# Kernel optimization log

Hardware: AMD Instinct MI355X
Metric: run time of the kernel (lower is better)

## Reference

```python
import jax, jax.numpy as jnp
import numpy as np
from jax import lax

B, N, C = 8, 16384, 128
HEADS, FF, KS = 8, 3.0, 5
HD = C // HEADS

def setup_inputs() -> dict:
    key = jax.random.key(0)
    ks = jax.random.split(key, 10)
    r = lambda k, s, sc=0.02: jax.random.normal(k, s, dtype=jnp.float32) * sc
    return {
        "x": jax.random.normal(ks[0], (B, N, C), dtype=jnp.float32),
        "Wq": r(ks[1], (C, C)),
        "Wkv": r(ks[2], (C, C)),
        "Wproj": r(ks[3], (C, C)),
        "bproj": jnp.zeros((C,), jnp.float32),
        "w_g": jax.random.normal(ks[4], (C, 1), dtype=jnp.float32),
        "scale": r(ks[5], (1, 1, C), 0.1),
        "pos_enc": r(ks[6], (1, N, C), 0.02),
        "dwc_w": r(ks[7], (HD, 1, KS, KS), 0.1),
        "dwc_b": jnp.zeros((HD,), jnp.float32),
        "H": 128,
        "W": 128,
    }

def _l2(a, axis):
    return jnp.sqrt(jnp.sum(a * a, axis=axis, keepdims=True))

def reference(x, Wq, Wkv, Wproj, bproj, w_g, scale, pos_enc, dwc_w, dwc_b, H, W):
    b, n_tok, c = x.shape
    scale_factor = HD ** (-0.5)
    q = x @ Wq.T                      # (B,N,C)
    k = x @ Wkv.T + pos_enc           # (B,N,C)  sr_ratio=1 path
    s = jax.nn.softplus(scale)
    q = (jax.nn.relu(q) + 1e-6) / s
    k = (jax.nn.relu(k) + 1e-6) / s
    qn, kn = _l2(q, -1), _l2(k, -1)
    q = q ** FF
    k = k ** FF
    q = q / _l2(q, -1) * qn
    k = k / _l2(k, -1) * kn
    A = (q @ w_g) * scale_factor      # (B,N,1)
    A = A / jnp.maximum(_l2(A, 1), 1e-12)  # F.normalize over dim=1
    G = jnp.sum(A * q, axis=1)        # (B,C)
    xg = G[:, None, :] * k            # (B,N,C)
    qh = q.reshape(b, n_tok, HEADS, HD).transpose(0, 2, 1, 3)  # (B,h,N,d)
    kh = k.reshape(b, n_tok, HEADS, HD).transpose(0, 2, 1, 3)
    z = 1.0 / (jnp.einsum('bhnd,bhd->bhn', qh, kh.mean(axis=2)) + 1e-6)
    xh = xg.reshape(b, n_tok, HEADS, HD).transpose(0, 2, 1, 3) * z[..., None]
    xo = xh.transpose(0, 2, 1, 3).reshape(b, n_tok, c)
    # faithful second transpose+reshape (memory reinterpretation in the source)
    xo = xo.transpose(0, 2, 1).reshape(b, n_tok, c)
    kimg = kh.reshape(b * HEADS, H, W, HD).transpose(0, 3, 1, 2)  # (B*h,d,H,W)
    pad = KS // 2
    conv = lax.conv_general_dilated(kimg, dwc_w, (1, 1), [(pad, pad), (pad, pad)],
                                    dimension_numbers=('NCHW', 'OIHW', 'NCHW'),
                                    feature_group_count=HD)
    conv = conv + dwc_b[None, :, None, None]
    xo = xo + conv.reshape(b, c, n_tok).transpose(0, 2, 1)
    return xo @ Wproj.T + bproj
```

## Files before the change

### kernel.cpp

```cpp
#include <hip/hip_runtime.h>
#include <hip/hip_bf16.h>

#define BB 8
#define NN 16384
#define CC 128

typedef __attribute__((ext_vector_type(8))) short bf16x8;
typedef __attribute__((ext_vector_type(4))) short short4v;
typedef __attribute__((ext_vector_type(4))) float f32x4;

__device__ __forceinline__ unsigned short f2bf(float f) {
    union { float f; unsigned u; } v; v.f = f;
    unsigned r = v.u + 0x7fffu + ((v.u >> 16) & 1u);
    return (unsigned short)(r >> 16);
}
__device__ __forceinline__ float bf2f(unsigned short h) {
    union { unsigned u; float f; } v; v.u = ((unsigned)h) << 16;
    return v.f;
}
__device__ __forceinline__ void split_trunc(float f, short& hi, short& lo) {
    union { float f; unsigned u; } v; v.f = f;
    const unsigned short hu = (unsigned short)(v.u >> 16);
    union { unsigned u; float f; } hf; hf.u = ((unsigned)hu) << 16;
    union { float f; unsigned u; } r; r.f = f - hf.f;
    hi = (short)hu;
    lo = (short)(r.u >> 16);
}

__global__ __launch_bounds__(256) void wprep_kernel(
    const float* __restrict__ Wq, const float* __restrict__ Wkv,
    const float* __restrict__ Wp, const float* __restrict__ scale,
    unsigned short* __restrict__ whi, unsigned short* __restrict__ wlo,
    float* __restrict__ sps)
{
    const int bid = blockIdx.x;
    if (bid == 48) {
        if (threadIdx.x < 128)
            sps[threadIdx.x] = 1.f / log1pf(expf(scale[threadIdx.x]));
        return;
    }
    const int mat = bid >> 4;
    const float* src = (mat == 0) ? Wq : ((mat == 1) ? Wkv : Wp);
    const int off = (bid & 15) * 1024 + threadIdx.x * 4;
    const float4 v = *(const float4*)(src + off);
    float f[4] = {v.x, v.y, v.z, v.w};
    short4v hv, lv;
#pragma unroll
    for (int j = 0; j < 4; ++j) {
        short h, lo2;
        split_trunc(f[j], h, lo2);
        hv[j] = h; lv[j] = lo2;
    }
    *(short4v*)(whi + mat * 16384 + off) = hv;
    *(short4v*)(wlo + mat * 16384 + off) = lv;
}

__global__ __launch_bounds__(256, 1) void qk_mfma_kernel(
    const float* __restrict__ x, const unsigned short* __restrict__ whi,
    const unsigned short* __restrict__ wlo, const float* __restrict__ w_g,
    const float* __restrict__ sps, const float* __restrict__ pos_enc,
    unsigned short* __restrict__ qout, unsigned short* __restrict__ kout,
    unsigned short* __restrict__ ktout, float* __restrict__ partial)
{
    __shared__ __align__(16) char wsm[131072];
    __shared__ float wpart[4][257];
    __shared__ float apl[128];

    const int tid  = threadIdx.x;
    const int w    = tid >> 6;
    const int l    = tid & 63;
    const int blk  = blockIdx.x;
    const int tok0 = blk * 128;
    const int tokb = (blk & 127) * 128;

    bf16x8 xh[2][4], xl[2][4];
#pragma unroll
    for (int n = 0; n < 2; ++n) {
        const int r = w * 32 + n * 16 + (l & 15);
        const float* rowp = x + (tok0 + r) * 128 + (l >> 4) * 8;
#pragma unroll
        for (int kt = 0; kt < 4; ++kt) {
            const f32x4 a = *(const f32x4*)(rowp + kt * 32);
            const f32x4 b = *(const f32x4*)(rowp + kt * 32 + 4);
            const float f[8] = {a[0], a[1], a[2], a[3], b[0], b[1], b[2], b[3]};
            bf16x8 hv, lv;
#pragma unroll
            for (int j = 0; j < 8; ++j) {
                short h, lo2;
                split_trunc(f[j], h, lo2);
                hv[j] = h; lv[j] = lo2;
            }
            xh[n][kt] = hv; xl[n][kt] = lv;
        }
    }

#pragma unroll
    for (int it = 0; it < 32; ++it) {
        const int flat = it * 256 + tid;
        const int arr  = flat >> 11;
        const int c    = (flat >> 4) & 127;
        const int g    = flat & 15;
        const unsigned short* src = ((arr & 1) ? wlo : whi)
                                  + ((arr >> 1) ? 16384 : 0) + c * 128 + g * 8;
        const int dst = arr * 32768 + c * 256 + ((g * 16) ^ ((c & 7) << 4));
        *(bf16x8*)(wsm + dst) = *(const bf16x8*)src;
    }
    __syncthreads();

    const int crow = (l >> 4) * 4;
    f32x4 accq[8][2], acck[8][2];
#pragma unroll
    for (int m = 0; m < 8; ++m)
#pragma unroll
        for (int n = 0; n < 2; ++n) { accq[m][n] = (f32x4)0.f; acck[m][n] = (f32x4)0.f; }

#pragma unroll
    for (int m = 0; m < 8; ++m) {
        const int c = m * 16 + (l & 15);
        const int sw = (c & 7) << 4;
        bf16x8 aqh[4], aql[4], akh[4], akl[4];
#pragma unroll
        for (int kt = 0; kt < 4; ++kt) {
            const int fo = c * 256 + ((kt * 64 + (l >> 4) * 16) ^ sw);
            aqh[kt] = *(const bf16x8*)(wsm + fo);
            aql[kt] = *(const bf16x8*)(wsm + 32768 + fo);
            akh[kt] = *(const bf16x8*)(wsm + 65536 + fo);
            akl[kt] = *(const bf16x8*)(wsm + 98304 + fo);
        }
#pragma unroll
        for (int n = 0; n < 2; ++n)
#pragma unroll
            for (int kt = 0; kt < 4; ++kt) {
                accq[m][n] = __builtin_amdgcn_mfma_f32_16x16x32_bf16(aqh[kt], xh[n][kt], accq[m][n], 0, 0, 0);
                acck[m][n] = __builtin_amdgcn_mfma_f32_16x16x32_bf16(akh[kt], xh[n][kt], acck[m][n], 0, 0, 0);
                accq[m][n] = __builtin_amdgcn_mfma_f32_16x16x32_bf16(aqh[kt], xl[n][kt], accq[m][n], 0, 0, 0);
                acck[m][n] = __builtin_amdgcn_mfma_f32_16x16x32_bf16(akh[kt], xl[n][kt], acck[m][n], 0, 0, 0);
                accq[m][n] = __builtin_amdgcn_mfma_f32_16x16x32_bf16(aql[kt], xh[n][kt], accq[m][n], 0, 0, 0);
                acck[m][n] = __builtin_amdgcn_mfma_f32_16x16x32_bf16(akl[kt], xh[n][kt], acck[m][n], 0, 0, 0);
            }
    }
    __syncthreads();

    {
#pragma unroll
        for (int m = 0; m < 8; ++m) {
            const float4 is4 = *(const float4*)(sps + m * 16 + crow);
            const float is[4] = {is4.x, is4.y, is4.z, is4.w};
#pragma unroll
            for (int n = 0; n < 2; ++n)
#pragma unroll
                for (int j = 0; j < 4; ++j)
                    accq[m][n][j] = (fmaxf(accq[m][n][j], 0.f) + 1e-6f) * is[j];
        }
        float fqn[2];
#pragma unroll
        for (int n = 0; n < 2; ++n) {
            float s2 = 0.f, s6 = 0.f;
#pragma unroll
            for (int m = 0; m < 8; ++m)
#pragma unroll
                for (int j = 0; j < 4; ++j) {
                    const float v = accq[m][n][j], v2 = v * v;
                    s2 += v2; s6 += v2 * v2 * v2;
                }
            s2 += __shfl_xor(s2, 16); s6 += __shfl_xor(s6, 16);
            s2 += __shfl_xor(s2, 32); s6 += __shfl_xor(s6, 32);
            fqn[n] = sqrtf(s2 / s6);
        }
#pragma unroll
        for (int m = 0; m < 8; ++m)
#pragma unroll
            for (int n = 0; n < 2; ++n)
#pragma unroll
                for (int j = 0; j < 4; ++j) {
                    const float v = accq[m][n][j];
                    accq[m][n][j] = v * v * v * fqn[n];
                }
        float d0 = 0.f, d1 = 0.f;
#pragma unroll
        for (int m = 0; m < 8; ++m) {
            const float4 wgv = *(const float4*)(w_g + m * 16 + crow);
#pragma unroll
            for (int j = 0; j < 4; ++j) {
                const float wg = (j == 0) ? wgv.x : (j == 1) ? wgv.y : (j == 2) ? wgv.z : wgv.w;
                d0 += accq[m][0][j] * wg;
                d1 += accq[m][1][j] * wg;
            }
        }
        d0 += __shfl_xor(d0, 16); d0 += __shfl_xor(d0, 32);
        d1 += __shfl_xor(d1, 16); d1 += __shfl_xor(d1, 32);
        const float ap0 = 0.25f * d0, ap1 = 0.25f * d1;

        float ssa = ap0 * ap0 + ap1 * ap1;
        ssa += __shfl_xor(ssa, 1); ssa += __shfl_xor(ssa, 2);
        ssa += __shfl_xor(ssa, 4); ssa += __shfl_xor(ssa, 8);
        if (l == 0) wpart[w][256] = ssa;
        if (l < 16) { apl[w * 32 + l] = ap0; apl[w * 32 + 16 + l] = ap1; }

        float g4[4] = {0.f, 0.f, 0.f, 0.f};
#pragma unroll
        for (int n = 0; n < 2; ++n) {
            const int t = l & 15;
            const int rb = w * 8192 + t * 512;
#pragma unroll
            for (int m = 0; m < 8; ++m) {
                const int ad = rb + (((m * 16 + crow) * 4) ^ ((t & 7) << 4));
                *(f32x4*)(wsm + ad) = accq[m][n];
            }
            asm volatile("s_waitcnt lgkmcnt(0)" ::: "memory");
#pragma unroll
            for (int j = 0; j < 8; ++j) {
                const int fid = j * 64 + l;
                const int row = fid >> 5;
                const int c4  = fid & 31;
                const int rb3 = w * 8192 + row * 512;
                const f32x4 v = *(f32x4*)(wsm + rb3 + ((c4 * 16) ^ ((row & 7) << 4)));
                const float apv = apl[w * 32 + n * 16 + row];
                short4v qv;
#pragma unroll
                for (int i = 0; i < 4; ++i) {
                    g4[i] += apv * v[i];
                    qv[i] = (short)f2bf(v[i]);
                }
                *(short4v*)(qout + (tok0 + w * 32 + n * 16 + row) * 128 + c4 * 4) = qv;
            }
        }
#pragma unroll
        for (int i = 0; i < 4; ++i) g4[i] += __shfl_xor(g4[i], 32);
        if (l < 32) {
#pragma unroll
            for (int i = 0; i < 4; ++i) wpart[w][(l & 31) * 4 + i] = g4[i];
        }
    }

    {
#pragma unroll
        for (int m = 0; m < 8; ++m) {
            const float4 is4 = *(const float4*)(sps + m * 16 + crow);
            const float is[4] = {is4.x, is4.y, is4.z, is4.w};
#pragma unroll
            for (int n = 0; n < 2; ++n) {
                const int t = tokb + w * 32 + n * 16 + (l & 15);
                const float4 p = *(const float4*)(pos_enc + t * 128 + m * 16 + crow);
                const float pe[4] = {p.x, p.y, p.z, p.w};
#pragma unroll
                for (int j = 0; j < 4; ++j)
                    acck[m][n][j] = (fmaxf(acck[m][n][j] + pe[j], 0.f) + 1e-6f) * is[j];
            }
        }
        float fkn[2];
#pragma unroll
        for (int n = 0; n < 2; ++n) {
            float s2 = 0.f, s6 = 0.f;
#pragma unroll
            for (int m = 0; m < 8; ++m)
#pragma unroll
                for (int j = 0; j < 4; ++j) {
                    const float v = acck[m][n][j], v2 = v * v;
                    s2 += v2; s6 += v2 * v2 * v2;
                }
            s2 += __shfl_xor(s2, 16); s6 += __shfl_xor(s6, 16);
            s2 += __shfl_xor(s2, 32); s6 += __shfl_xor(s6, 32);
            fkn[n] = sqrtf(s2 / s6);
        }
#pragma unroll
        for (int m = 0; m < 8; ++m)
#pragma unroll
            for (int n = 0; n < 2; ++n)
#pragma unroll
                for (int j = 0; j < 4; ++j) {
                    const float v = acck[m][n][j];
                    acck[m][n][j] = v * v * v * fkn[n];
                }
        float ks4[4] = {0.f, 0.f, 0.f, 0.f};
#pragma unroll
        for (int n = 0; n < 2; ++n) {
            const int t = l & 15;
            const int rb = w * 8192 + t * 512;
#pragma unroll
            for (int m = 0; m < 8; ++m) {
                const int ad = rb + (((m * 16 + crow) * 4) ^ ((t & 7) << 4));
                *(f32x4*)(wsm + ad) = acck[m][n];
            }
            asm volatile("s_waitcnt lgkmcnt(0)" ::: "memory");
#pragma unroll
            for (int j = 0; j < 8; ++j) {
                const int fid = j * 64 + l;
                const int row = fid >> 5;
                const int c4  = fid & 31;
                const int rb3 = w * 8192 + row * 512;
                const f32x4 v = *(f32x4*)(wsm + rb3 + ((c4 * 16) ^ ((row & 7) << 4)));
                short4v kv;
#pragma unroll
                for (int i = 0; i < 4; ++i) {
                    ks4[i] += v[i];
                    kv[i] = (short)f2bf(v[i]);
                }
                *(short4v*)(kout + (tok0 + w * 32 + n * 16 + row) * 128 + c4 * 4) = kv;
            }
        }
#pragma unroll
        for (int i = 0; i < 4; ++i) ks4[i] += __shfl_xor(ks4[i], 32);
        if (l < 32) {
#pragma unroll
            for (int i = 0; i < 4; ++i) wpart[w][128 + (l & 31) * 4 + i] = ks4[i];
        }
    }

    __syncthreads();
#pragma unroll
    for (int m = 0; m < 8; ++m)
#pragma unroll
        for (int n = 0; n < 2; ++n)
#pragma unroll
            for (int j = 0; j < 4; ++j) {
                const int ch = m * 16 + crow + j;
                const int tl = w * 32 + n * 16 + (l & 15);
                *(unsigned short*)(wsm + ch * 264 + tl * 2) = f2bf(acck[m][n][j]);
            }
    __syncthreads();
    {
        const int bb = blk >> 7;
        unsigned* ktp = (unsigned*)ktout;
#pragma unroll
        for (int it = 0; it < 32; ++it) {
            const int idx = it * 256 + tid;
            const int row = idx >> 6;
            const int col = idx & 63;
            const unsigned v = *(unsigned*)(wsm + row * 264 + col * 4);
            ktp[(size_t)(bb * 128 + row) * 8192 + (blk & 127) * 64 + col] = v;
        }
    }

    __syncthreads();
    float* pblk = partial + blk * 257;
    if (tid < 128) {
        pblk[tid] = wpart[0][tid] + wpart[1][tid] + wpart[2][tid] + wpart[3][tid];
        pblk[128 + tid] = wpart[0][128 + tid] + wpart[1][128 + tid] +
                          wpart[2][128 + tid] + wpart[3][128 + tid];
    } else if (tid == 128) {
        pblk[256] = wpart[0][256] + wpart[1][256] + wpart[2][256] + wpart[3][256];
    }
}

__global__ __launch_bounds__(256) void reduce_kernel(
    const float* __restrict__ partial, float* __restrict__ G,
    float* __restrict__ kbar)
{
    const int b = blockIdx.x;
    const int tid = threadIdx.x;
    __shared__ float tmp[4];

    float ssa = (tid < 128) ? partial[(b * 128 + tid) * 257 + 256] : 0.f;
#pragma unroll
    for (int o = 32; o >= 1; o >>= 1) ssa += __shfl_xor(ssa, o);
    if ((tid & 63) == 0) tmp[tid >> 6] = ssa;
    __syncthreads();
    const float anorm = fmaxf(sqrtf(tmp[0] + tmp[1] + tmp[2] + tmp[3]), 1e-12f);
    const float inv_a = 1.f / anorm;

    if (tid < 128) {
        float g = 0.f;
        for (int t = 0; t < 128; ++t)
            g += partial[(b * 128 + t) * 257 + tid];
        G[b * 128 + tid] = g * inv_a;
    } else {
        const int c2 = tid - 128;
        float s = 0.f;
        for (int t = 0; t < 128; ++t)
            s += partial[(b * 128 + t) * 257 + 128 + c2];
        kbar[b * 128 + c2] = s * (1.f / 16384.f);
    }
}

__global__ __launch_bounds__(256) void z_kernel(
    const unsigned short* __restrict__ q, const float* __restrict__ kbar,
    float* __restrict__ z)
{
    const int bid = blockIdx.x;
    const int b   = bid >> 8;
    const int tg  = bid & 255;
    const int tid = threadIdx.x;
    const int t   = tid >> 2;
    const int qt  = tid & 3;
    const int tok = tg * 64 + t;

    const unsigned short* qp = q + ((size_t)b * NN + tok) * 128 + qt * 32;
    const float* kb = kbar + b * 128 + qt * 32;

    float dot0 = 0.f, dot1 = 0.f;
#pragma unroll
    for (int c = 0; c < 4; ++c) {
        const short4v q4a = *(const short4v*)(qp + c * 8);
        const short4v q4b = *(const short4v*)(qp + c * 8 + 4);
        const float4 k4a = *(const float4*)(kb + c * 8);
        const float4 k4b = *(const float4*)(kb + c * 8 + 4);
        float d = bf2f((unsigned short)q4a[0]) * k4a.x + bf2f((unsigned short)q4a[1]) * k4a.y +
                  bf2f((unsigned short)q4a[2]) * k4a.z + bf2f((unsigned short)q4a[3]) * k4a.w +
                  bf2f((unsigned short)q4b[0]) * k4b.x + bf2f((unsigned short)q4b[1]) * k4b.y +
                  bf2f((unsigned short)q4b[2]) * k4b.z + bf2f((unsigned short)q4b[3]) * k4b.w;
        if (c < 2) dot0 += d; else dot1 += d;
    }
    z[((size_t)b * 8 + qt * 2) * NN + tok]     = 1.f / (dot0 + 1e-6f);
    z[((size_t)b * 8 + qt * 2 + 1) * NN + tok] = 1.f / (dot1 + 1e-6f);
}

__global__ __launch_bounds__(256, 2) void scp_kernel(
    float* __restrict__ out, const unsigned short* __restrict__ kbuf,
    const unsigned short* __restrict__ kt, const float* __restrict__ z,
    const float* __restrict__ G,
    const unsigned short* __restrict__ whi, const unsigned short* __restrict__ wlo,
    const float* __restrict__ bp, const float* __restrict__ dwc_w,
    const float* __restrict__ dwc_b)
{
    __shared__ __align__(16) char smem[65536];
    __shared__ float wct[25][16];
    __shared__ float bi[16];
    __shared__ float Gs;

    const int tid  = threadIdx.x;
    const int bid0 = blockIdx.x;
    const int bid  = (bid0 & 7) * 128 + (bid0 >> 3);
    const int cc   = bid & 127;
    const int b    = bid >> 7;
    const int n0   = bid * 128;

    for (int i = tid; i < 400; i += 256)
        wct[i >> 4][i & 15] = dwc_w[(i & 15) * 25 + (i >> 4)];
    if (tid < 16) bi[tid] = dwc_b[tid];
    if (tid == 0) Gs = G[b * 128 + cc];
    __syncthreads();

    const int l  = tid & 31;
    const int xg = tid >> 5;
    const int dbase = (l & 3) * 4;

    float4 acc[16];
#pragma unroll
    for (int i = 0; i < 16; ++i) acc[i] = make_float4(0.f, 0.f, 0.f, 0.f);

#pragma unroll
    for (int dy = 0; dy < 5; ++dy) {
        const int yy = cc + dy - 2;
        if (yy < 0 || yy > 127) continue;
        const unsigned short* rowb = kbuf + (b * NN + yy * 128) * CC + l * 4;
        float4 rowv[20];
#pragma unroll
        for (int xi = 0; xi < 20; ++xi) {
            const int xx = xg * 16 - 2 + xi;
            if (xx >= 0 && xx < 128) {
                const short4v kv4 = *(const short4v*)(rowb + xx * CC);
                rowv[xi] = make_float4(bf2f((unsigned short)kv4[0]),
                                       bf2f((unsigned short)kv4[1]),
                                       bf2f((unsigned short)kv4[2]),
                                       bf2f((unsigned short)kv4[3]));
            } else {
                rowv[xi] = make_float4(0.f, 0.f, 0.f, 0.f);
            }
        }
#pragma unroll
        for (int dx = 0; dx < 5; ++dx) {
            const float4 wv = *(const float4*)(&wct[dy * 5 + dx][dbase]);
#pragma unroll
            for (int i = 0; i < 16; ++i) {
                acc[i].x += wv.x * rowv[i + dx].x;
                acc[i].y += wv.y * rowv[i + dx].y;
                acc[i].z += wv.z * rowv[i + dx].z;
                acc[i].w += wv.w * rowv[i + dx].w;
            }
        }
    }

    const float Gcc = Gs;
    const unsigned short* kub = kt + ((size_t)b * 128 + cc) * NN;
    const float* zr = z + ((size_t)b * 8 + (cc >> 4)) * NN;
    const float4 b4 = *(const float4*)(&bi[dbase]);
#pragma unroll
    for (int i = 0; i < 16; ++i) {
        const int r = xg * 16 + i;
        const int toks = r * 128 + l * 4;
        const short4v ku4 = *(const short4v*)(kub + toks);
        const float4 z4 = *(const float4*)(zr + toks);
        const float zz[4] = {z4.x, z4.y, z4.z, z4.w};
        float f[4];
        const float av[4] = {acc[i].x, acc[i].y, acc[i].z, acc[i].w};
        const float bv[4] = {b4.x, b4.y, b4.z, b4.w};
#pragma unroll
        for (int c = 0; c < 4; ++c)
            f[c] = Gcc * bf2f((unsigned short)ku4[c]) * zz[c] + av[c] + bv[c];
        short4v hv, lv;
#pragma unroll
        for (int j = 0; j < 4; ++j) {
            short h, lo2;
            split_trunc(f[j], h, lo2);
            hv[j] = h; lv[j] = lo2;
        }
        const int ad = r * 256 + (((l >> 1) * 16) ^ ((r & 7) << 4)) + (l & 1) * 8;
        *(short4v*)(smem + ad) = hv;
        *(short4v*)(smem + 32768 + ad) = lv;
    }
    __syncthreads();

    const int w  = tid >> 6;
    const int ll = tid & 63;
    bf16x8 xh[2][4], xl[2][4];
    {
        const int lg16 = (ll >> 4) * 16;
#pragma unroll
        for (int n = 0; n < 2; ++n) {
            const int r = w * 32 + n * 16 + (ll & 15);
            const int rb = r * 256;
            const int sw = (r & 7) << 4;
#pragma unroll
            for (int kt2 = 0; kt2 < 4; ++kt2) {
                const int ad = rb + ((kt2 * 64 + lg16) ^ sw);
                xh[n][kt2] = *(bf16x8*)(smem + ad);
                xl[n][kt2] = *(bf16x8*)(smem + 32768 + ad);
            }
        }
    }
    const int crow = (ll >> 4) * 4;
    f32x4 pacc[8][2];
#pragma unroll
    for (int m = 0; m < 8; ++m)
#pragma unroll
        for (int n = 0; n < 2; ++n) pacc[m][n] = (f32x4)0.f;

#pragma unroll
    for (int m = 0; m < 8; ++m) {
        const int c = m * 16 + (ll & 15);
        bf16x8 ah[4], al[4];
#pragma unroll
        for (int kt2 = 0; kt2 < 4; ++kt2) {
            const int off = 32768 + c * 128 + kt2 * 32 + (ll >> 4) * 8;
            ah[kt2] = *(const bf16x8*)(whi + off);
            al[kt2] = *(const bf16x8*)(wlo + off);
        }
#pragma unroll
        for (int n = 0; n < 2; ++n)
#pragma unroll
            for (int kt2 = 0; kt2 < 4; ++kt2) {
                pacc[m][n] = __builtin_amdgcn_mfma_f32_16x16x32_bf16(ah[kt2], xh[n][kt2], pacc[m][n], 0, 0, 0);
                pacc[m][n] = __builtin_amdgcn_mfma_f32_16x16x32_bf16(ah[kt2], xl[n][kt2], pacc[m][n], 0, 0, 0);
                pacc[m][n] = __builtin_amdgcn_mfma_f32_16x16x32_bf16(al[kt2], xh[n][kt2], pacc[m][n], 0, 0, 0);
            }
    }

#pragma unroll
    for (int m = 0; m < 8; ++m) {
        const float4 bv = *(const float4*)(bp + m * 16 + crow);
        const float bb[4] = {bv.x, bv.y, bv.z, bv.w};
#pragma unroll
        for (int n = 0; n < 2; ++n)
#pragma unroll
            for (int j = 0; j < 4; ++j) pacc[m][n][j] += bb[j];
    }
    __syncthreads();
#pragma unroll
    for (int n = 0; n < 2; ++n) {
        const int t = n * 16 + (ll & 15);
        const int rb = w * 8192 + (t & 15) * 512 + ((t >= 16) ? 32768 : 0);
#pragma unroll
        for (int m = 0; m < 8; ++m) {
            const int ad = rb + (((m * 16 + crow) * 4) ^ ((t & 7) << 4));
            *(f32x4*)(smem + ad) = pacc[m][n];
        }
    }
    asm volatile("s_waitcnt lgkmcnt(0)" ::: "memory");
#pragma unroll
    for (int j = 0; j < 16; ++j) {
        const int fid = j * 64 + ll;
        const int row = fid >> 5;
        const int c4 = fid & 31;
        const int rb = w * 8192 + (row & 15) * 512 + ((row >= 16) ? 32768 : 0);
        const f32x4 v = *(f32x4*)(smem + rb + ((c4 * 16) ^ ((row & 7) << 4)));
        *(f32x4*)(out + (n0 + w * 32 + row) * 128 + c4 * 4) = v;
    }
}

extern "C" void kernel_launch(void* const* d_in, const int* in_sizes, int n_in,
                              void* d_out, int out_size, void* d_ws, size_t ws_size,
                              hipStream_t stream)
{
    const float* x       = (const float*)d_in[0];
    const float* Wq      = (const float*)d_in[1];
    const float* Wkv     = (const float*)d_in[2];
    const float* Wproj   = (const float*)d_in[3];
    const float* bproj   = (const float*)d_in[4];
    const float* w_g     = (const float*)d_in[5];
    const float* scale   = (const float*)d_in[6];
    const float* pos_enc = (const float*)d_in[7];
    const float* dwc_w   = (const float*)d_in[8];
    const float* dwc_b   = (const float*)d_in[9];
    float* out = (float*)d_out;

    char* ws = (char*)d_ws;
    unsigned short* qbuf = (unsigned short*)(ws);
    unsigned short* kbuf = (unsigned short*)(ws + 33554432);
    unsigned short* ktbuf= (unsigned short*)(ws + 67108864);
    float* partial = (float*)(ws + 100663296);
    float* G       = (float*)(ws + 101715968);
    float* kbar    = (float*)(ws + 101720064);
    unsigned short* whi = (unsigned short*)(ws + 101724160);
    unsigned short* wlo = (unsigned short*)(ws + 101822464);
    float* sps     = (float*)(ws + 101920768);
    float* zbuf    = (float*)(ws + 101921280);

    wprep_kernel<<<dim3(49), dim3(256), 0, stream>>>(
        Wq, Wkv, Wproj, scale, whi, wlo, sps);
    qk_mfma_kernel<<<dim3(1024), dim3(256), 0, stream>>>(
        x, whi, wlo, w_g, sps, pos_enc, qbuf, kbuf, ktbuf, partial);
    reduce_kernel<<<dim3(8), dim3(256), 0, stream>>>(partial, G, kbar);
    z_kernel<<<dim3(2048), dim3(256), 0, stream>>>(qbuf, kbar, zbuf);
    scp_kernel<<<dim3(1024), dim3(256), 0, stream>>>(
        out, kbuf, ktbuf, zbuf, G, whi, wlo, bproj, dwc_w, dwc_b);
}
```

Baseline: 190.8 us.

## Halve LDS and registers in fused conv+proj kernel, drop low bf16 activation split

The fused depthwise-conv/projection kernel now rounds activations to a single bf16 instead of a hi/lo split, which halves LDS staging and removes one of three MFMA passes. The conv runs in two halves of 8 rows to cut register pressure, the output staging reuses a 32 KB buffer in two passes, and launch bounds are raised to 3 blocks per CU. These changes target occupancy and MFMA count. In exchange, activations lose precision (only the weight is split), which may affect accuracy tolerance.

```diff
diff --git a/kernel.cpp b/kernel.cpp
--- a/kernel.cpp
+++ b/kernel.cpp
@@ -405,7 +405,7 @@
     z[((size_t)b * 8 + qt * 2 + 1) * NN + tok] = 1.f / (dot1 + 1e-6f);
 }
 
-__global__ __launch_bounds__(256, 2) void scp_kernel(
+__global__ __launch_bounds__(256, 3) void scp_kernel(
     float* __restrict__ out, const unsigned short* __restrict__ kbuf,
     const unsigned short* __restrict__ kt, const float* __restrict__ z,
     const float* __restrict__ G,
@@ -413,7 +413,7 @@
     const float* __restrict__ bp, const float* __restrict__ dwc_w,
     const float* __restrict__ dwc_b)
 {
-    __shared__ __align__(16) char smem[65536];
+    __shared__ __align__(16) char smem[32768];
     __shared__ float wct[25][16];
     __shared__ float bi[16];
     __shared__ float Gs;
@@ -435,75 +435,73 @@
     const int xg = tid >> 5;
     const int dbase = (l & 3) * 4;
 
-    float4 acc[16];
-#pragma unroll
-    for (int i = 0; i < 16; ++i) acc[i] = make_float4(0.f, 0.f, 0.f, 0.f);
-
-#pragma unroll
-    for (int dy = 0; dy < 5; ++dy) {
-        const int yy = cc + dy - 2;
-        if (yy < 0 || yy > 127) continue;
-        const unsigned short* rowb = kbuf + (b * NN + yy * 128) * CC + l * 4;
-        float4 rowv[20];
-#pragma unroll
-        for (int xi = 0; xi < 20; ++xi) {
-            const int xx = xg * 16 - 2 + xi;
-            if (xx >= 0 && xx < 128) {
-                const short4v kv4 = *(const short4v*)(rowb + xx * CC);
-                rowv[xi] = make_float4(bf2f((unsigned short)kv4[0]),
-                                       bf2f((unsigned short)kv4[1]),
-                                       bf2f((unsigned short)kv4[2]),
-                                       bf2f((unsigned short)kv4[3]));
-            } else {
-                rowv[xi] = make_float4(0.f, 0.f, 0.f, 0.f);
-            }
-        }
-#pragma unroll
-        for (int dx = 0; dx < 5; ++dx) {
-            const float4 wv = *(const float4*)(&wct[dy * 5 + dx][dbase]);
-#pragma unroll
-            for (int i = 0; i < 16; ++i) {
-                acc[i].x += wv.x * rowv[i + dx].x;
-                acc[i].y += wv.y * rowv[i + dx].y;
-                acc[i].z += wv.z * rowv[i + dx].z;
-                acc[i].w += wv.w * rowv[i + dx].w;
-            }
-        }
-    }
-
     const float Gcc = Gs;
     const unsigned short* kub = kt + ((size_t)b * 128 + cc) * NN;
     const float* zr = z + ((size_t)b * 8 + (cc >> 4)) * NN;
     const float4 b4 = *(const float4*)(&bi[dbase]);
-#pragma unroll
-    for (int i = 0; i < 16; ++i) {
-        const int r = xg * 16 + i;
-        const int toks = r * 128 + l * 4;
-        const short4v ku4 = *(const short4v*)(kub + toks);
-        const float4 z4 = *(const float4*)(zr + toks);
-        const float zz[4] = {z4.x, z4.y, z4.z, z4.w};
-        float f[4];
-        const float av[4] = {acc[i].x, acc[i].y, acc[i].z, acc[i].w};
-        const float bv[4] = {b4.x, b4.y, b4.z, b4.w};
-#pragma unroll
-        for (int c = 0; c < 4; ++c)
-            f[c] = Gcc * bf2f((unsigned short)ku4[c]) * zz[c] + av[c] + bv[c];
-        short4v hv, lv;
-#pragma unroll
-        for (int j = 0; j < 4; ++j) {
-            short h, lo2;
-            split_trunc(f[j], h, lo2);
-            hv[j] = h; lv[j] = lo2;
-        }
-        const int ad = r * 256 + (((l >> 1) * 16) ^ ((r & 7) << 4)) + (l & 1) * 8;
-        *(short4v*)(smem + ad) = hv;
-        *(short4v*)(smem + 32768 + ad) = lv;
+    const float bv[4] = {b4.x, b4.y, b4.z, b4.w};
+
+#pragma unroll
+    for (int h = 0; h < 2; ++h) {
+        float4 acc[8];
+#pragma unroll
+        for (int i = 0; i < 8; ++i) acc[i] = make_float4(0.f, 0.f, 0.f, 0.f);
+
+#pragma unroll
+        for (int dy = 0; dy < 5; ++dy) {
+            const int yy = cc + dy - 2;
+            if (yy < 0 || yy > 127) continue;
+            const unsigned short* rowb = kbuf + (b * NN + yy * 128) * CC + l * 4;
+            float4 rowv[12];
+#pragma unroll
+            for (int xi = 0; xi < 12; ++xi) {
+                const int xx = xg * 16 + h * 8 - 2 + xi;
+                if (xx >= 0 && xx < 128) {
+                    const short4v kv4 = *(const short4v*)(rowb + xx * CC);
+                    rowv[xi] = make_float4(bf2f((unsigned short)kv4[0]),
+                                           bf2f((unsigned short)kv4[1]),
+                                           bf2f((unsigned short)kv4[2]),
+                                           bf2f((unsigned short)kv4[3]));
+                } else {
+                    rowv[xi] = make_float4(0.f, 0.f, 0.f, 0.f);
+                }
+            }
+#pragma unroll
+            for (int dx = 0; dx < 5; ++dx) {
+                const float4 wv = *(const float4*)(&wct[dy * 5 + dx][dbase]);
+#pragma unroll
+                for (int i = 0; i < 8; ++i) {
+                    acc[i].x += wv.x * rowv[i + dx].x;
+                    acc[i].y += wv.y * rowv[i + dx].y;
+                    acc[i].z += wv.z * rowv[i + dx].z;
+                    acc[i].w += wv.w * rowv[i + dx].w;
+                }
+            }
+        }
+
+#pragma unroll
+        for (int i = 0; i < 8; ++i) {
+            const int r = xg * 16 + h * 8 + i;
+            const int toks = r * 128 + l * 4;
+            const short4v ku4 = *(const short4v*)(kub + toks);
+            const float4 z4 = *(const float4*)(zr + toks);
+            const float zz[4] = {z4.x, z4.y, z4.z, z4.w};
+            const float av[4] = {acc[i].x, acc[i].y, acc[i].z, acc[i].w};
+            short4v hv;
+#pragma unroll
+            for (int c = 0; c < 4; ++c) {
+                const float f = Gcc * bf2f((unsigned short)ku4[c]) * zz[c] + av[c] + bv[c];
+                hv[c] = (short)f2bf(f);
+            }
+            const int ad = r * 256 + (((l >> 1) * 16) ^ ((r & 7) << 4)) + (l & 1) * 8;
+            *(short4v*)(smem + ad) = hv;
+        }
     }
     __syncthreads();
 
     const int w  = tid >> 6;
     const int ll = tid & 63;
-    bf16x8 xh[2][4], xl[2][4];
+    bf16x8 xh[2][4];
     {
         const int lg16 = (ll >> 4) * 16;
 #pragma unroll
@@ -512,11 +510,8 @@
             const int rb = r * 256;
             const int sw = (r & 7) << 4;
 #pragma unroll
-            for (int kt2 = 0; kt2 < 4; ++kt2) {
-                const int ad = rb + ((kt2 * 64 + lg16) ^ sw);
-                xh[n][kt2] = *(bf16x8*)(smem + ad);
-                xl[n][kt2] = *(bf16x8*)(smem + 32768 + ad);
-            }
+            for (int kt2 = 0; kt2 < 4; ++kt2)
+                xh[n][kt2] = *(bf16x8*)(smem + rb + ((kt2 * 64 + lg16) ^ sw));
         }
     }
     const int crow = (ll >> 4) * 4;
@@ -541,15 +536,14 @@
 #pragma unroll
             for (int kt2 = 0; kt2 < 4; ++kt2) {
                 pacc[m][n] = __builtin_amdgcn_mfma_f32_16x16x32_bf16(ah[kt2], xh[n][kt2], pacc[m][n], 0, 0, 0);
-                pacc[m][n] = __builtin_amdgcn_mfma_f32_16x16x32_bf16(ah[kt2], xl[n][kt2], pacc[m][n], 0, 0, 0);
                 pacc[m][n] = __builtin_amdgcn_mfma_f32_16x16x32_bf16(al[kt2], xh[n][kt2], pacc[m][n], 0, 0, 0);
             }
     }
 
 #pragma unroll
     for (int m = 0; m < 8; ++m) {
-        const float4 bv = *(const float4*)(bp + m * 16 + crow);
-        const float bb[4] = {bv.x, bv.y, bv.z, bv.w};
+        const float4 bq = *(const float4*)(bp + m * 16 + crow);
+        const float bb[4] = {bq.x, bq.y, bq.z, bq.w};
 #pragma unroll
         for (int n = 0; n < 2; ++n)
 #pragma unroll
@@ -558,23 +552,23 @@
     __syncthreads();
 #pragma unroll
     for (int n = 0; n < 2; ++n) {
-        const int t = n * 16 + (ll & 15);
-        const int rb = w * 8192 + (t & 15) * 512 + ((t >= 16) ? 32768 : 0);
+        const int t = ll & 15;
+        const int rb = w * 8192 + t * 512;
 #pragma unroll
         for (int m = 0; m < 8; ++m) {
             const int ad = rb + (((m * 16 + crow) * 4) ^ ((t & 7) << 4));
             *(f32x4*)(smem + ad) = pacc[m][n];
         }
-    }
-    asm volatile("s_waitcnt lgkmcnt(0)" ::: "memory");
-#pragma unroll
-    for (int j = 0; j < 16; ++j) {
-        const int fid = j * 64 + ll;
-        const int row = fid >> 5;
-        const int c4 = fid & 31;
-        const int rb = w * 8192 + (row & 15) * 512 + ((row >= 16) ? 32768 : 0);
-        const f32x4 v = *(f32x4*)(smem + rb + ((c4 * 16) ^ ((row & 7) << 4)));
-        *(f32x4*)(out + (n0 + w * 32 + row) * 128 + c4 * 4) = v;
+        asm volatile("s_waitcnt lgkmcnt(0)" ::: "memory");
+#pragma unroll
+        for (int j = 0; j < 8; ++j) {
+            const int fid = j * 64 + ll;
+            const int row = fid >> 5;
+            const int c4  = fid & 31;
+            const int rb3 = w * 8192 + row * 512;
+            const f32x4 v = *(f32x4*)(smem + rb3 + ((c4 * 16) ^ ((row & 7) << 4)));
+            *(f32x4*)(out + (n0 + w * 32 + n * 16 + row) * 128 + c4 * 4) = v;
+        }
     }
 }
 
```

New measurement: 194.9 us. +2.1%, slower.
